# Optimization experiments

Hardware: AMD Instinct MI355X
Metric: run time of the kernel (lower is better)

Reference implementation:

```python
import jax, jax.numpy as jnp
import numpy as np

B, F0, D = 1024, 32, 32
HID = [128, 128, 128]


def setup_inputs() -> dict:
    key = jax.random.key(0)
    ks = jax.random.split(key, 4)
    inputs = jax.random.normal(ks[0], (B, F0, D), dtype=jnp.float32)
    # glorot-like init for conv filters, flattened to (F0*Fk, H)
    def glorot(k, fan_in, fan_out):
        lim = np.sqrt(6.0 / (fan_in + fan_out)).astype(np.float32)
        return jax.random.uniform(k, (fan_in, fan_out), dtype=jnp.float32, minval=-lim, maxval=lim)
    W0 = glorot(ks[1], F0 * F0, HID[0])
    W1 = glorot(ks[2], F0 * HID[0], HID[1])
    W2 = glorot(ks[3], F0 * HID[1], HID[2])
    b0 = jnp.zeros((HID[0],), dtype=jnp.float32)
    b1 = jnp.zeros((HID[1],), dtype=jnp.float32)
    b2 = jnp.zeros((HID[2],), dtype=jnp.float32)
    return {"inputs": inputs, "W0": W0, "W1": W1, "W2": W2,
            "b0": b0, "b1": b1, "b2": b2,
            "field_size": F0, "embedding_size": D}


def _cin_layer(x0, state, W, b):
    # x0: (B, F0, D), state: (B, Fk, D)
    bsz, f0, d = x0.shape
    fk = state.shape[1]
    # per-embedding-dim outer product; flatten (f0, fk) row-major to match
    # tf reshape of matmul(state_split_0, state_split_k^T)
    z = jnp.einsum('bfd,bgd->bdfg', x0, state).reshape(bsz, d, f0 * fk)
    h = z @ W + b  # (B, D, H); 1x1 conv1d == matmul over f0*fk
    # activation is linear (identity)
    return jnp.transpose(h, (0, 2, 1))  # (B, H, D)


def reference(inputs, W0, W1, W2, b0, b1, b2, field_size, embedding_size):
    x0 = inputs.reshape(-1, field_size, embedding_size)
    state = x0
    outputs = []
    for W, b in ((W0, b0), (W1, b1), (W2, b2)):
        fm = _cin_layer(x0, state, W, b)
        state = fm          # skip=False: state and output are the full map
        outputs.append(fm)
    # concat over field axis, sum over embedding dim -> (B, sum(H))
    return jnp.sum(jnp.concatenate(outputs, axis=1), axis=-1)
```

## Files before the change

kernel.cpp:

```cpp
#include <hip/hip_runtime.h>
#include <hip/hip_bf16.h>


typedef __attribute__((ext_vector_type(8))) short short8;
typedef __attribute__((ext_vector_type(8))) __bf16 bf16x8;
typedef __attribute__((ext_vector_type(16))) float f32x16;
typedef __attribute__((ext_vector_type(4))) unsigned short u16x4;

#define DEVINL static __device__ __forceinline__

DEVINL unsigned short f2bf_rne(float f) {
  unsigned int u = __builtin_bit_cast(unsigned int, f);
  unsigned int r = u + 0x7fffu + ((u >> 16) & 1u);
  return (unsigned short)(r >> 16);
}

DEVINL void gload_lds16(const void* g, void* l) {
  __builtin_amdgcn_global_load_lds(
      (const __attribute__((address_space(1))) unsigned int*)g,
      (__attribute__((address_space(3))) unsigned int*)l, 16, 0, 0);
}

template <typename V>
DEVINL auto mfma_32x32x16_bf16(V a, V b, f32x16 c, int)
    -> decltype(__builtin_amdgcn_mfma_f32_32x32x16_bf16(a, b, c, 0, 0, 0)) {
  return __builtin_amdgcn_mfma_f32_32x32x16_bf16(a, b, c, 0, 0, 0);
}
template <typename V>
DEVINL f32x16 mfma_32x32x16_bf16(V a, V b, f32x16 c, long) {
  return __builtin_amdgcn_mfma_f32_32x32x16_bf16(
      __builtin_bit_cast(bf16x8, a), __builtin_bit_cast(bf16x8, b), c, 0, 0, 0);
}
DEVINL f32x16 mfma_bf16(short8 a, short8 b, f32x16 c) {
  return mfma_32x32x16_bf16(a, b, c, 0);
}

__global__ void pack_w_kernel(const float* __restrict__ W0,
                              const float* __restrict__ W1,
                              const float* __restrict__ W2,
                              unsigned short* __restrict__ Wt) {
  __shared__ float tile[8][132];
  const int u = blockIdx.x;
  const float* W; int FK, f, kb, base;
  if (u < 128)      { W = W0; FK = 32;  f = u >> 2;         kb = u & 3;          base = 0; }
  else if (u < 640) { W = W1; FK = 128; f = (u - 128) >> 4; kb = (u - 128) & 15; base = 131072; }
  else              { W = W2; FK = 128; f = (u - 640) >> 4; kb = (u - 640) & 15; base = 655360; }
  const int t = threadIdx.x;
#pragma unroll
  for (int i = 0; i < 4; ++i) {
    const int e = t + i * 256;
    const int kk = e >> 7, h = e & 127;
    tile[kk][h] = W[(f * FK + kb * 8 + kk) * 128 + h];
  }
  __syncthreads();
  unsigned short* dst = Wt + base + f * (FK / 8) * 1024 + kb * 1024;
  const int h = t >> 1;
  const int j0 = (t & 1) * 4;
  u16x4 v;
  v.x = f2bf_rne(tile[j0 + 0][h]);
  v.y = f2bf_rne(tile[j0 + 1][h]);
  v.z = f2bf_rne(tile[j0 + 2][h]);
  v.w = f2bf_rne(tile[j0 + 3][h]);
  *(u16x4*)&dst[t * 4] = v;
}

template <int KQ, int LAYER>
DEVINL void run_layer(const unsigned short* __restrict__ WtL,
                      const float* __restrict__ bias,
                      const float* x0l,
                      float* __restrict__ outp, int outoff,
                      unsigned int* SB, unsigned short* wlds,
                      int w, int lane, int mrow, int npair, int l31, int half) {
  __syncthreads();

  constexpr int NC   = (KQ == 8) ? 32 : 16;
  constexpr int CU16 = (KQ == 8) ? 16384 : 8192;
  constexpr int LP   = (KQ == 8) ? 4 : 2;

  auto stage = [&](int c, int buf) {
#pragma unroll
    for (int j = 0; j < LP; ++j) {
      const int off = (w * LP + j) * 512;
      gload_lds16(WtL + (size_t)c * CU16 + off + lane * 8,
                  wlds + buf * CU16 + off);
    }
  };

  stage(0, 0);

  int4 sfr[2][KQ];
  const int rb = npair * 64;
#pragma unroll
  for (int nt = 0; nt < 2; ++nt) {
    const int r = rb + nt * 32 + l31;
#pragma unroll
    for (int kq = 0; kq < KQ; ++kq) {
      const int row0 = kq * 8 + half * 4;
      int4 v;
      v.x = (int)SB[(row0 + 0) * 128 + r];
      v.y = (int)SB[(row0 + 1) * 128 + r];
      v.z = (int)SB[(row0 + 2) * 128 + r];
      v.w = (int)SB[(row0 + 3) * 128 + r];
      sfr[nt][kq] = v;
    }
  }

  f32x16 zv;
#pragma unroll
  for (int e = 0; e < 16; ++e) zv[e] = 0.f;
  f32x16 outacc[2] = {zv, zv};

  __syncthreads();

  const int hrow = mrow * 32 + l31;
  const int fro = half * 1024 + hrow * 8;
  const int xb0 = (npair * 2 + 0) * 1024 + l31;
  const int xb1 = (npair * 2 + 1) * 1024 + l31;

#pragma unroll 1
  for (int c = 0; c < NC; ++c) {
    if (c + 1 < NC) stage(c + 1, (c + 1) & 1);
    const unsigned short* fb = wlds + (c & 1) * CU16;

    if constexpr (KQ == 8) {
      const float xs0 = x0l[xb0 + c * 32];
      const float xs1 = x0l[xb1 + c * 32];
      f32x16 Y0, Y1;
#pragma unroll
      for (int kq = 0; kq < 8; ++kq) {
        const short8 wv =
            *(const short8*)&fb[(kq >> 2) * 8192 + (kq & 3) * 2048 + fro];
        const short8 s0 = __builtin_bit_cast(short8, sfr[0][kq]);
        const short8 s1 = __builtin_bit_cast(short8, sfr[1][kq]);
        Y0 = mfma_bf16(wv, s0, kq == 0 ? zv : Y0);
        Y1 = mfma_bf16(wv, s1, kq == 0 ? zv : Y1);
      }
#pragma unroll
      for (int e = 0; e < 16; ++e) {
        outacc[0][e] += xs0 * Y0[e];
        outacc[1][e] += xs1 * Y1[e];
      }
    } else {
      const float xA0 = x0l[xb0 + (2 * c + 0) * 32];
      const float xA1 = x0l[xb1 + (2 * c + 0) * 32];
      const float xB0 = x0l[xb0 + (2 * c + 1) * 32];
      const float xB1 = x0l[xb1 + (2 * c + 1) * 32];
      const short8 s00 = __builtin_bit_cast(short8, sfr[0][0]);
      const short8 s01 = __builtin_bit_cast(short8, sfr[0][1]);
      const short8 s10 = __builtin_bit_cast(short8, sfr[1][0]);
      const short8 s11 = __builtin_bit_cast(short8, sfr[1][1]);
      short8 wv[4];
#pragma unroll
      for (int i = 0; i < 4; ++i)
        wv[i] = *(const short8*)&fb[i * 2048 + fro];
      f32x16 Y0 = mfma_bf16(wv[0], s00, zv);
      Y0 = mfma_bf16(wv[1], s01, Y0);
      f32x16 Y1 = mfma_bf16(wv[0], s10, zv);
      Y1 = mfma_bf16(wv[1], s11, Y1);
      f32x16 Z0 = mfma_bf16(wv[2], s00, zv);
      Z0 = mfma_bf16(wv[3], s01, Z0);
      f32x16 Z1 = mfma_bf16(wv[2], s10, zv);
      Z1 = mfma_bf16(wv[3], s11, Z1);
#pragma unroll
      for (int e = 0; e < 16; ++e) {
        outacc[0][e] += xA0 * Y0[e] + xB0 * Z0[e];
        outacc[1][e] += xA1 * Y1[e] + xB1 * Z1[e];
      }
    }
    __syncthreads();
  }

  float bv[16];
#pragma unroll
  for (int e = 0; e < 16; ++e)
    bv[e] = bias[mrow * 32 + (e & 3) + 8 * (e >> 2) + 4 * half];

  if constexpr (LAYER < 2) {
#pragma unroll
    for (int nt = 0; nt < 2; ++nt) {
      const int r = rb + nt * 32 + l31;
#pragma unroll
      for (int g = 0; g < 4; ++g) {
        const int h2 = mrow * 16 + 4 * g + 2 * half;
        const float v0 = outacc[nt][4 * g + 0] + bv[4 * g + 0];
        const float v1 = outacc[nt][4 * g + 1] + bv[4 * g + 1];
        const float v2 = outacc[nt][4 * g + 2] + bv[4 * g + 2];
        const float v3 = outacc[nt][4 * g + 3] + bv[4 * g + 3];
        SB[h2 * 128 + r] =
            (unsigned)f2bf_rne(v0) | ((unsigned)f2bf_rne(v1) << 16);
        SB[(h2 + 1) * 128 + r] =
            (unsigned)f2bf_rne(v2) | ((unsigned)f2bf_rne(v3) << 16);
      }
    }
  }

#pragma unroll
  for (int nt = 0; nt < 2; ++nt) {
    float sv[16];
#pragma unroll
    for (int e = 0; e < 16; ++e) {
      float v = outacc[nt][e];
      v += __shfl_xor(v, 1);
      v += __shfl_xor(v, 2);
      v += __shfl_xor(v, 4);
      v += __shfl_xor(v, 8);
      v += __shfl_xor(v, 16);
      sv[e] = v + 32.0f * bv[e];
    }
    if (l31 == 0) {
      const int b = npair * 2 + nt;
#pragma unroll
      for (int g = 0; g < 4; ++g) {
        const int h = mrow * 32 + 8 * g + 4 * half;
        float4 o = {sv[4 * g + 0], sv[4 * g + 1], sv[4 * g + 2], sv[4 * g + 3]};
        *(float4*)&outp[b * 384 + outoff + h] = o;
      }
    }
  }
}

DEVINL void run_layer2_fast(const unsigned short* __restrict__ WtL,
                            const float* __restrict__ bias,
                            const float* x0l,
                            float* __restrict__ outp,
                            unsigned int* SB, int wgb0,
                            int w, int l31, int half, int tid) {
  __syncthreads();

  f32x16 zv;
#pragma unroll
  for (int e = 0; e < 16; ++e) zv[e] = 0.f;

  const int bw = w >> 1, gh = w & 1;
  short8 a1[2];
  {
    const float* xr = &x0l[bw * 1024 + l31 * 32];
#pragma unroll
    for (int kq = 0; kq < 2; ++kq) {
      const int d0 = kq * 16 + half * 8;
      union { short8 v; unsigned short u[8]; } t;
#pragma unroll
      for (int j = 0; j < 8; ++j) t.u[j] = f2bf_rne(xr[d0 + j]);
      a1[kq] = t.v;
    }
  }
  short8 bfr[2][2];
#pragma unroll
  for (int nt = 0; nt < 2; ++nt) {
    const int g = gh * 64 + nt * 32 + l31;
    const unsigned int* row = &SB[(g >> 1) * 128 + bw * 32];
    const int sh = (g & 1) * 16;
#pragma unroll
    for (int kq = 0; kq < 2; ++kq) {
      const int d0 = kq * 16 + half * 8;
      union { short8 v; unsigned short u[8]; } t;
#pragma unroll
      for (int j = 0; j < 8; ++j)
        t.u[j] = (unsigned short)(row[d0 + j] >> sh);
      bfr[nt][kq] = t.v;
    }
  }
  f32x16 ua[2];
#pragma unroll
  for (int nt = 0; nt < 2; ++nt) {
    ua[nt] = mfma_bf16(a1[0], bfr[nt][0], zv);
    ua[nt] = mfma_bf16(a1[1], bfr[nt][1], ua[nt]);
  }
  __syncthreads();

  unsigned short* U16 = (unsigned short*)SB;
#pragma unroll
  for (int nt = 0; nt < 2; ++nt) {
    const int g = gh * 64 + nt * 32 + l31;
#pragma unroll
    for (int reg = 0; reg < 16; ++reg) {
      const int f = (reg & 3) + 8 * (reg >> 2) + 4 * half;
      const int k = f * 128 + g;
      U16[(k >> 1) * 8 + bw * 2 + (k & 1)] = f2bf_rne(ua[nt][reg]);
    }
  }
  __syncthreads();

  const int mt = w & 3, kh = w >> 2;
  const char* gb = (const char*)WtL +
                   (size_t)(half * 2048 + (mt * 32 + l31) * 16);
  const int bl = l31 & 3;

  auto ldq2 = [&](short8* wv, int q) {
#pragma unroll
    for (int i = 0; i < 4; ++i)
      wv[i] = *(const short8*)(gb + (size_t)q * 16384 + i * 4096);
  };
  auto breadq = [&](short8* bv, int q) {
#pragma unroll
    for (int i = 0; i < 4; ++i) {
      const int row0 = (q * 4 + i) * 8 + half * 4;
      int4 v;
      v.x = (int)SB[(row0 + 0) * 4 + bl];
      v.y = (int)SB[(row0 + 1) * 4 + bl];
      v.z = (int)SB[(row0 + 2) * 4 + bl];
      v.w = (int)SB[(row0 + 3) * 4 + bl];
      bv[i] = __builtin_bit_cast(short8, v);
    }
  };

  f32x16 acc0 = zv, acc1 = zv;
  short8 qa[4], qb[4], Ba[4], Bb[4];
  const int q0 = kh * 32;
  ldq2(qa, q0);
  breadq(Ba, q0);
#pragma unroll 1
  for (int qq = 0; qq < 16; ++qq) {
    const int q = q0 + 2 * qq;
    ldq2(qb, q + 1);
    breadq(Bb, q + 1);
#pragma unroll
    for (int i = 0; i < 4; ++i) acc0 = mfma_bf16(qa[i], Ba[i], acc0);
    if (qq < 15) {
      ldq2(qa, q + 2);
      breadq(Ba, q + 2);
    }
#pragma unroll
    for (int i = 0; i < 4; ++i) acc1 = mfma_bf16(qb[i], Bb[i], acc1);
  }
#pragma unroll
  for (int e = 0; e < 16; ++e) acc0[e] += acc1[e];

  __syncthreads();

  float* P = (float*)SB;
  if (l31 < 4) {
#pragma unroll
    for (int reg = 0; reg < 16; ++reg) {
      const int h = mt * 32 + (reg & 3) + 8 * (reg >> 2) + 4 * half;
      P[(l31 * 128 + h) * 2 + kh] = acc0[reg];
    }
  }
  __syncthreads();
  {
    const int b = tid >> 7, h = tid & 127;
    const float v = P[tid * 2] + P[tid * 2 + 1] + 32.0f * bias[h];
    outp[b * 384 + 256 + h] = v;
  }
}

__global__ __launch_bounds__(512, 1) void cin_kernel(
    const float* __restrict__ x0g, const unsigned short* __restrict__ Wt,
    const float* __restrict__ b0, const float* __restrict__ b1,
    const float* __restrict__ b2, float* __restrict__ out) {
  __shared__ unsigned int SB[64 * 128];
  __shared__ __align__(16) float x0l[4096];
  __shared__ __align__(16) unsigned short wlds[32768];

  const int t = threadIdx.x;
  const int lane = t & 63;
  const int w = t >> 6;
  const int mrow = w & 3;
  const int npair = w >> 2;
  const int l31 = lane & 31, half = lane >> 5;
  const int wgb0 = blockIdx.x * 4;

  const float* xsrc = x0g + (size_t)wgb0 * 1024;
#pragma unroll
  for (int c = 0; c < 2; ++c) {
    const int chunk = w * 2 + c;
    gload_lds16(xsrc + chunk * 256 + lane * 4, x0l + chunk * 256);
  }
#pragma unroll
  for (int s = 0; s < 4; ++s) {
    const int i = t + s * 512;
    const int r = i & 127, g2 = i >> 7;
    const float* p = &x0g[(wgb0 + (r >> 5)) * 1024 + (2 * g2) * 32 + (r & 31)];
    SB[g2 * 128 + r] =
        (unsigned)f2bf_rne(p[0]) | ((unsigned)f2bf_rne(p[32]) << 16);
  }

  float* outp = out + (size_t)wgb0 * 384;
  run_layer<2, 0>(Wt, b0, x0l, outp, 0, SB, wlds, w, lane, mrow, npair, l31,
                  half);
  run_layer<8, 1>(Wt + 131072, b1, x0l, outp, 128, SB, wlds, w, lane, mrow,
                  npair, l31, half);
  run_layer2_fast(Wt + 655360, b2, x0l, outp, SB, wgb0, w, l31, half, t);
}

extern "C" void kernel_launch(void* const* d_in, const int* in_sizes, int n_in,
                              void* d_out, int out_size, void* d_ws, size_t ws_size,
                              hipStream_t stream) {
  (void)in_sizes; (void)n_in; (void)out_size; (void)ws_size;
  const float* x0 = (const float*)d_in[0];
  const float* W0 = (const float*)d_in[1];
  const float* W1 = (const float*)d_in[2];
  const float* W2 = (const float*)d_in[3];
  const float* b0 = (const float*)d_in[4];
  const float* b1 = (const float*)d_in[5];
  const float* b2 = (const float*)d_in[6];
  unsigned short* Wt = (unsigned short*)d_ws;

  pack_w_kernel<<<1152, 256, 0, stream>>>(W0, W1, W2, Wt);
  cin_kernel<<<256, 512, 0, stream>>>(x0, Wt, b0, b1, b2, (float*)d_out);
}
```

Measured before the change: 143.3 us.

## Triple-buffer weight staging with one barrier per chunk and uniform chunk size

Weight chunks move from double buffering to a three-slot LDS ring, with two chunks prefetched ahead. Each iteration waits on vmcnt and hits a single barrier, where before it had a trailing __syncthreads. The small-K layers now use 16K-element chunks covering four fields each, which halves their chunk count and barrier overhead. The cost is a larger LDS footprint, and the hand-written vmcnt counts depend on the exact number of outstanding loads.

```diff
diff --git a/kernel.cpp b/kernel.cpp
--- a/kernel.cpp
+++ b/kernel.cpp
@@ -73,9 +73,9 @@
                       int w, int lane, int mrow, int npair, int l31, int half) {
   __syncthreads();
 
-  constexpr int NC   = (KQ == 8) ? 32 : 16;
-  constexpr int CU16 = (KQ == 8) ? 16384 : 8192;
-  constexpr int LP   = (KQ == 8) ? 4 : 2;
+  constexpr int NC = (KQ == 8) ? 32 : 8;
+  constexpr int CU16 = 16384;
+  constexpr int LP = 4;
 
   auto stage = [&](int c, int buf) {
 #pragma unroll
@@ -87,6 +87,7 @@
   };
 
   stage(0, 0);
+  stage(1, 1);
 
   int4 sfr[2][KQ];
   const int rb = npair * 64;
@@ -110,26 +111,19 @@
   for (int e = 0; e < 16; ++e) zv[e] = 0.f;
   f32x16 outacc[2] = {zv, zv};
 
-  __syncthreads();
-
   const int hrow = mrow * 32 + l31;
   const int fro = half * 1024 + hrow * 8;
   const int xb0 = (npair * 2 + 0) * 1024 + l31;
   const int xb1 = (npair * 2 + 1) * 1024 + l31;
 
-#pragma unroll 1
-  for (int c = 0; c < NC; ++c) {
-    if (c + 1 < NC) stage(c + 1, (c + 1) & 1);
-    const unsigned short* fb = wlds + (c & 1) * CU16;
-
+  auto doChunk = [&](int c, const unsigned short* fb) {
     if constexpr (KQ == 8) {
       const float xs0 = x0l[xb0 + c * 32];
       const float xs1 = x0l[xb1 + c * 32];
       f32x16 Y0, Y1;
 #pragma unroll
       for (int kq = 0; kq < 8; ++kq) {
-        const short8 wv =
-            *(const short8*)&fb[(kq >> 2) * 8192 + (kq & 3) * 2048 + fro];
+        const short8 wv = *(const short8*)&fb[kq * 2048 + fro];
         const short8 s0 = __builtin_bit_cast(short8, sfr[0][kq]);
         const short8 s1 = __builtin_bit_cast(short8, sfr[1][kq]);
         Y0 = mfma_bf16(wv, s0, kq == 0 ? zv : Y0);
@@ -141,34 +135,40 @@
         outacc[1][e] += xs1 * Y1[e];
       }
     } else {
-      const float xA0 = x0l[xb0 + (2 * c + 0) * 32];
-      const float xA1 = x0l[xb1 + (2 * c + 0) * 32];
-      const float xB0 = x0l[xb0 + (2 * c + 1) * 32];
-      const float xB1 = x0l[xb1 + (2 * c + 1) * 32];
       const short8 s00 = __builtin_bit_cast(short8, sfr[0][0]);
       const short8 s01 = __builtin_bit_cast(short8, sfr[0][1]);
       const short8 s10 = __builtin_bit_cast(short8, sfr[1][0]);
       const short8 s11 = __builtin_bit_cast(short8, sfr[1][1]);
-      short8 wv[4];
-#pragma unroll
-      for (int i = 0; i < 4; ++i)
-        wv[i] = *(const short8*)&fb[i * 2048 + fro];
-      f32x16 Y0 = mfma_bf16(wv[0], s00, zv);
-      Y0 = mfma_bf16(wv[1], s01, Y0);
-      f32x16 Y1 = mfma_bf16(wv[0], s10, zv);
-      Y1 = mfma_bf16(wv[1], s11, Y1);
-      f32x16 Z0 = mfma_bf16(wv[2], s00, zv);
-      Z0 = mfma_bf16(wv[3], s01, Z0);
-      f32x16 Z1 = mfma_bf16(wv[2], s10, zv);
-      Z1 = mfma_bf16(wv[3], s11, Z1);
-#pragma unroll
-      for (int e = 0; e < 16; ++e) {
-        outacc[0][e] += xA0 * Y0[e] + xB0 * Z0[e];
-        outacc[1][e] += xA1 * Y1[e] + xB1 * Z1[e];
+#pragma unroll
+      for (int ff = 0; ff < 4; ++ff) {
+        const int f = 4 * c + ff;
+        const float xs0 = x0l[xb0 + f * 32];
+        const float xs1 = x0l[xb1 + f * 32];
+        const short8 w0 = *(const short8*)&fb[(2 * ff + 0) * 2048 + fro];
+        const short8 w1 = *(const short8*)&fb[(2 * ff + 1) * 2048 + fro];
+        f32x16 Y0 = mfma_bf16(w0, s00, zv);
+        Y0 = mfma_bf16(w1, s01, Y0);
+        f32x16 Y1 = mfma_bf16(w0, s10, zv);
+        Y1 = mfma_bf16(w1, s11, Y1);
+#pragma unroll
+        for (int e = 0; e < 16; ++e) {
+          outacc[0][e] += xs0 * Y0[e];
+          outacc[1][e] += xs1 * Y1[e];
+        }
       }
     }
-    __syncthreads();
-  }
+  };
+
+#pragma unroll 1
+  for (int c = 0; c < NC - 1; ++c) {
+    asm volatile("s_waitcnt vmcnt(4)" ::: "memory");
+    __builtin_amdgcn_s_barrier();
+    if (c + 2 < NC) stage(c + 2, (c + 2) % 3);
+    doChunk(c, wlds + (c % 3) * CU16);
+  }
+  asm volatile("s_waitcnt vmcnt(0)" ::: "memory");
+  __builtin_amdgcn_s_barrier();
+  doChunk(NC - 1, wlds + ((NC - 1) % 3) * CU16);
 
   float bv[16];
 #pragma unroll
@@ -350,7 +350,7 @@
     const float* __restrict__ b2, float* __restrict__ out) {
   __shared__ unsigned int SB[64 * 128];
   __shared__ __align__(16) float x0l[4096];
-  __shared__ __align__(16) unsigned short wlds[32768];
+  __shared__ __align__(16) unsigned short wlds[49152];
 
   const int t = threadIdx.x;
   const int lane = t & 63;
```

Measured after the change: 144.2 us. About the same (+0.6%).

## Split CIN K-dimension across 16 waves with LDS reduction, drop weight LDS staging

Applied to the files above, without the earlier changes.

Doubles the workgroup to 1024 threads and splits each layer's reduction dimension across two wave groups, combining partial accumulators through a new LDS reduction buffer. Weights are now read directly from global memory into registers with a two-field software prefetch, replacing the double-buffered LDS staging and its per-chunk barriers. Layer 2 is likewise re-partitioned over 16 waves with a four-way K split. This aims to raise latency hiding and per-CU parallelism, at the cost of extra reduction traffic and reliance on cache bandwidth for weight loads.

```diff
diff --git a/kernel.cpp b/kernel.cpp
--- a/kernel.cpp
+++ b/kernel.cpp
@@ -64,38 +64,24 @@
   *(u16x4*)&dst[t * 4] = v;
 }
 
-template <int KQ, int LAYER>
+template <int KQG, int FS, int LAYER>
 DEVINL void run_layer(const unsigned short* __restrict__ WtL,
                       const float* __restrict__ bias,
                       const float* x0l,
                       float* __restrict__ outp, int outoff,
-                      unsigned int* SB, unsigned short* wlds,
-                      int w, int lane, int mrow, int npair, int l31, int half) {
-  __syncthreads();
-
-  constexpr int NC   = (KQ == 8) ? 32 : 16;
-  constexpr int CU16 = (KQ == 8) ? 16384 : 8192;
-  constexpr int LP   = (KQ == 8) ? 4 : 2;
-
-  auto stage = [&](int c, int buf) {
-#pragma unroll
-    for (int j = 0; j < LP; ++j) {
-      const int off = (w * LP + j) * 512;
-      gload_lds16(WtL + (size_t)c * CU16 + off + lane * 8,
-                  wlds + buf * CU16 + off);
-    }
-  };
-
-  stage(0, 0);
-
-  int4 sfr[2][KQ];
+                      unsigned int* SB, float* red,
+                      int w, int lane, int mrow, int npair, int gs,
+                      int l31, int half) {
+  __syncthreads();
+
+  int4 sfr[2][KQG];
   const int rb = npair * 64;
 #pragma unroll
   for (int nt = 0; nt < 2; ++nt) {
     const int r = rb + nt * 32 + l31;
 #pragma unroll
-    for (int kq = 0; kq < KQ; ++kq) {
-      const int row0 = kq * 8 + half * 4;
+    for (int kq = 0; kq < KQG; ++kq) {
+      const int row0 = (gs * KQG + kq) * 8 + half * 4;
       int4 v;
       v.x = (int)SB[(row0 + 0) * 128 + r];
       v.y = (int)SB[(row0 + 1) * 128 + r];
@@ -110,65 +96,62 @@
   for (int e = 0; e < 16; ++e) zv[e] = 0.f;
   f32x16 outacc[2] = {zv, zv};
 
-  __syncthreads();
-
   const int hrow = mrow * 32 + l31;
-  const int fro = half * 1024 + hrow * 8;
+  const unsigned short* gb =
+      WtL + (size_t)(gs * KQG * 2048 + half * 1024 + hrow * 8);
   const int xb0 = (npair * 2 + 0) * 1024 + l31;
   const int xb1 = (npair * 2 + 1) * 1024 + l31;
 
+  auto ldf = [&](short8* wv, int f) {
+#pragma unroll
+    for (int i = 0; i < KQG; ++i)
+      wv[i] = *(const short8*)&gb[(size_t)f * FS + i * 2048];
+  };
+  auto doFld = [&](const short8* wv, float xs0, float xs1) {
+    f32x16 Y0, Y1;
+#pragma unroll
+    for (int i = 0; i < KQG; ++i) {
+      const short8 s0 = __builtin_bit_cast(short8, sfr[0][i]);
+      const short8 s1 = __builtin_bit_cast(short8, sfr[1][i]);
+      Y0 = mfma_bf16(wv[i], s0, i == 0 ? zv : Y0);
+      Y1 = mfma_bf16(wv[i], s1, i == 0 ? zv : Y1);
+    }
+#pragma unroll
+    for (int e = 0; e < 16; ++e) {
+      outacc[0][e] += xs0 * Y0[e];
+      outacc[1][e] += xs1 * Y1[e];
+    }
+  };
+
+  short8 wa[KQG], wb[KQG];
+  ldf(wa, 0);
+  ldf(wb, 1);
 #pragma unroll 1
-  for (int c = 0; c < NC; ++c) {
-    if (c + 1 < NC) stage(c + 1, (c + 1) & 1);
-    const unsigned short* fb = wlds + (c & 1) * CU16;
-
-    if constexpr (KQ == 8) {
-      const float xs0 = x0l[xb0 + c * 32];
-      const float xs1 = x0l[xb1 + c * 32];
-      f32x16 Y0, Y1;
-#pragma unroll
-      for (int kq = 0; kq < 8; ++kq) {
-        const short8 wv =
-            *(const short8*)&fb[(kq >> 2) * 8192 + (kq & 3) * 2048 + fro];
-        const short8 s0 = __builtin_bit_cast(short8, sfr[0][kq]);
-        const short8 s1 = __builtin_bit_cast(short8, sfr[1][kq]);
-        Y0 = mfma_bf16(wv, s0, kq == 0 ? zv : Y0);
-        Y1 = mfma_bf16(wv, s1, kq == 0 ? zv : Y1);
-      }
-#pragma unroll
-      for (int e = 0; e < 16; ++e) {
-        outacc[0][e] += xs0 * Y0[e];
-        outacc[1][e] += xs1 * Y1[e];
-      }
-    } else {
-      const float xA0 = x0l[xb0 + (2 * c + 0) * 32];
-      const float xA1 = x0l[xb1 + (2 * c + 0) * 32];
-      const float xB0 = x0l[xb0 + (2 * c + 1) * 32];
-      const float xB1 = x0l[xb1 + (2 * c + 1) * 32];
-      const short8 s00 = __builtin_bit_cast(short8, sfr[0][0]);
-      const short8 s01 = __builtin_bit_cast(short8, sfr[0][1]);
-      const short8 s10 = __builtin_bit_cast(short8, sfr[1][0]);
-      const short8 s11 = __builtin_bit_cast(short8, sfr[1][1]);
-      short8 wv[4];
-#pragma unroll
-      for (int i = 0; i < 4; ++i)
-        wv[i] = *(const short8*)&fb[i * 2048 + fro];
-      f32x16 Y0 = mfma_bf16(wv[0], s00, zv);
-      Y0 = mfma_bf16(wv[1], s01, Y0);
-      f32x16 Y1 = mfma_bf16(wv[0], s10, zv);
-      Y1 = mfma_bf16(wv[1], s11, Y1);
-      f32x16 Z0 = mfma_bf16(wv[2], s00, zv);
-      Z0 = mfma_bf16(wv[3], s01, Z0);
-      f32x16 Z1 = mfma_bf16(wv[2], s10, zv);
-      Z1 = mfma_bf16(wv[3], s11, Z1);
-#pragma unroll
-      for (int e = 0; e < 16; ++e) {
-        outacc[0][e] += xA0 * Y0[e] + xB0 * Z0[e];
-        outacc[1][e] += xA1 * Y1[e] + xB1 * Z1[e];
-      }
-    }
-    __syncthreads();
-  }
+  for (int f2 = 0; f2 < 16; ++f2) {
+    const int f = 2 * f2;
+    const float xs00 = x0l[xb0 + f * 32], xs01 = x0l[xb1 + f * 32];
+    const float xs10 = x0l[xb0 + (f + 1) * 32], xs11 = x0l[xb1 + (f + 1) * 32];
+    doFld(wa, xs00, xs01);
+    if (f2 < 15) ldf(wa, f + 2);
+    doFld(wb, xs10, xs11);
+    if (f2 < 15) ldf(wb, f + 3);
+  }
+
+  const int widx = w & 7;
+  if (gs) {
+#pragma unroll
+    for (int nt = 0; nt < 2; ++nt)
+#pragma unroll
+      for (int e = 0; e < 16; ++e)
+        red[((widx * 2 + nt) * 16 + e) * 64 + lane] = outacc[nt][e];
+  }
+  __syncthreads();
+  if (gs) return;
+#pragma unroll
+  for (int nt = 0; nt < 2; ++nt)
+#pragma unroll
+    for (int e = 0; e < 16; ++e)
+      outacc[nt][e] += red[((widx * 2 + nt) * 16 + e) * 64 + lane];
 
   float bv[16];
 #pragma unroll
@@ -223,7 +206,7 @@
                             const float* __restrict__ bias,
                             const float* x0l,
                             float* __restrict__ outp,
-                            unsigned int* SB, int wgb0,
+                            unsigned int* SB,
                             int w, int l31, int half, int tid) {
   __syncthreads();
 
@@ -231,7 +214,7 @@
 #pragma unroll
   for (int e = 0; e < 16; ++e) zv[e] = 0.f;
 
-  const int bw = w >> 1, gh = w & 1;
+  const int bw = w >> 2, gq = w & 3;
   short8 a1[2];
   {
     const float* xr = &x0l[bw * 1024 + l31 * 32];
@@ -244,10 +227,9 @@
       a1[kq] = t.v;
     }
   }
-  short8 bfr[2][2];
-#pragma unroll
-  for (int nt = 0; nt < 2; ++nt) {
-    const int g = gh * 64 + nt * 32 + l31;
+  short8 bfr[2];
+  {
+    const int g = gq * 32 + l31;
     const unsigned int* row = &SB[(g >> 1) * 128 + bw * 32];
     const int sh = (g & 1) * 16;
 #pragma unroll
@@ -257,26 +239,21 @@
 #pragma unroll
       for (int j = 0; j < 8; ++j)
         t.u[j] = (unsigned short)(row[d0 + j] >> sh);
-      bfr[nt][kq] = t.v;
-    }
-  }
-  f32x16 ua[2];
-#pragma unroll
-  for (int nt = 0; nt < 2; ++nt) {
-    ua[nt] = mfma_bf16(a1[0], bfr[nt][0], zv);
-    ua[nt] = mfma_bf16(a1[1], bfr[nt][1], ua[nt]);
-  }
+      bfr[kq] = t.v;
+    }
+  }
+  f32x16 ua = mfma_bf16(a1[0], bfr[0], zv);
+  ua = mfma_bf16(a1[1], bfr[1], ua);
   __syncthreads();
 
   unsigned short* U16 = (unsigned short*)SB;
-#pragma unroll
-  for (int nt = 0; nt < 2; ++nt) {
-    const int g = gh * 64 + nt * 32 + l31;
+  {
+    const int g = gq * 32 + l31;
 #pragma unroll
     for (int reg = 0; reg < 16; ++reg) {
       const int f = (reg & 3) + 8 * (reg >> 2) + 4 * half;
       const int k = f * 128 + g;
-      U16[(k >> 1) * 8 + bw * 2 + (k & 1)] = f2bf_rne(ua[nt][reg]);
+      U16[(k >> 1) * 8 + bw * 2 + (k & 1)] = f2bf_rne(ua[reg]);
     }
   }
   __syncthreads();
@@ -306,17 +283,17 @@
 
   f32x16 acc0 = zv, acc1 = zv;
   short8 qa[4], qb[4], Ba[4], Bb[4];
-  const int q0 = kh * 32;
+  const int q0 = kh * 16;
   ldq2(qa, q0);
   breadq(Ba, q0);
 #pragma unroll 1
-  for (int qq = 0; qq < 16; ++qq) {
+  for (int qq = 0; qq < 8; ++qq) {
     const int q = q0 + 2 * qq;
     ldq2(qb, q + 1);
     breadq(Bb, q + 1);
 #pragma unroll
     for (int i = 0; i < 4; ++i) acc0 = mfma_bf16(qa[i], Ba[i], acc0);
-    if (qq < 15) {
+    if (qq < 7) {
       ldq2(qa, q + 2);
       breadq(Ba, q + 2);
     }
@@ -333,42 +310,40 @@
 #pragma unroll
     for (int reg = 0; reg < 16; ++reg) {
       const int h = mt * 32 + (reg & 3) + 8 * (reg >> 2) + 4 * half;
-      P[(l31 * 128 + h) * 2 + kh] = acc0[reg];
-    }
-  }
-  __syncthreads();
-  {
+      P[(l31 * 128 + h) * 4 + kh] = acc0[reg];
+    }
+  }
+  __syncthreads();
+  if (tid < 512) {
     const int b = tid >> 7, h = tid & 127;
-    const float v = P[tid * 2] + P[tid * 2 + 1] + 32.0f * bias[h];
+    const float v = P[tid * 4 + 0] + P[tid * 4 + 1] + P[tid * 4 + 2] +
+                    P[tid * 4 + 3] + 32.0f * bias[h];
     outp[b * 384 + 256 + h] = v;
   }
 }
 
-__global__ __launch_bounds__(512, 1) void cin_kernel(
+__global__ __launch_bounds__(1024, 4) void cin_kernel(
     const float* __restrict__ x0g, const unsigned short* __restrict__ Wt,
     const float* __restrict__ b0, const float* __restrict__ b1,
     const float* __restrict__ b2, float* __restrict__ out) {
   __shared__ unsigned int SB[64 * 128];
   __shared__ __align__(16) float x0l[4096];
-  __shared__ __align__(16) unsigned short wlds[32768];
+  __shared__ __align__(16) float red[16384];
 
   const int t = threadIdx.x;
   const int lane = t & 63;
   const int w = t >> 6;
   const int mrow = w & 3;
-  const int npair = w >> 2;
+  const int npair = (w >> 2) & 1;
+  const int gs = w >> 3;
   const int l31 = lane & 31, half = lane >> 5;
   const int wgb0 = blockIdx.x * 4;
 
   const float* xsrc = x0g + (size_t)wgb0 * 1024;
-#pragma unroll
-  for (int c = 0; c < 2; ++c) {
-    const int chunk = w * 2 + c;
-    gload_lds16(xsrc + chunk * 256 + lane * 4, x0l + chunk * 256);
-  }
-#pragma unroll
-  for (int s = 0; s < 4; ++s) {
-    const int i = t + s * 512;
+  gload_lds16(xsrc + w * 256 + lane * 4, x0l + w * 256);
+#pragma unroll
+  for (int s = 0; s < 2; ++s) {
+    const int i = t + s * 1024;
     const int r = i & 127, g2 = i >> 7;
     const float* p = &x0g[(wgb0 + (r >> 5)) * 1024 + (2 * g2) * 32 + (r & 31)];
     SB[g2 * 128 + r] =
@@ -376,11 +351,11 @@
   }
 
   float* outp = out + (size_t)wgb0 * 384;
-  run_layer<2, 0>(Wt, b0, x0l, outp, 0, SB, wlds, w, lane, mrow, npair, l31,
-                  half);
-  run_layer<8, 1>(Wt + 131072, b1, x0l, outp, 128, SB, wlds, w, lane, mrow,
-                  npair, l31, half);
-  run_layer2_fast(Wt + 655360, b2, x0l, outp, SB, wgb0, w, l31, half, t);
+  run_layer<1, 4096, 0>(Wt, b0, x0l, outp, 0, SB, red, w, lane, mrow, npair,
+                        gs, l31, half);
+  run_layer<4, 16384, 1>(Wt + 131072, b1, x0l, outp, 128, SB, red, w, lane,
+                         mrow, npair, gs, l31, half);
+  run_layer2_fast(Wt + 655360, b2, x0l, outp, SB, w, l31, half, t);
 }
 
 extern "C" void kernel_launch(void* const* d_in, const int* in_sizes, int n_in,
@@ -397,5 +372,5 @@
   unsigned short* Wt = (unsigned short*)d_ws;
 
   pack_w_kernel<<<1152, 256, 0, stream>>>(W0, W1, W2, Wt);
-  cin_kernel<<<256, 512, 0, stream>>>(x0, Wt, b0, b1, b2, (float*)d_out);
-}
+  cin_kernel<<<256, 1024, 0, stream>>>(x0, Wt, b0, b1, b2, (float*)d_out);
+}
```

After: 379.7 us. 165% more time.
